# Kernel tuning notes

Measured on AMD Instinct MI355X. Metric: run time of the kernel, lower is better.

The kernel has to match this reference:

```python
import jax, jax.numpy as jnp
import numpy as np

N_NODES = 100000
N_EDGES = 1600000
DIM = 128
N_LAYERS = 3   # num_gc_layers
N_RES = 3      # residual VQ layers
N_CODE = 16    # codebook_size
N_GRAPHS = 512
BN_EPS = 1e-5
COMMIT_W = 0.25


def _l2norm(v):
    return v * jax.lax.rsqrt(jnp.sum(v * v, axis=-1, keepdims=True) + 1e-12)


def setup_inputs() -> dict:
    key = jax.random.key(0)
    ks = jax.random.split(key, 8)
    s = 0.05
    x = jax.random.normal(ks[0], (N_NODES, DIM), jnp.float32)
    edge_index = jax.random.randint(ks[1], (2, N_EDGES), 0, N_NODES)
    batch = jnp.sort(jax.random.randint(ks[2], (N_NODES,), 0, N_GRAPHS))
    W1 = jax.random.normal(ks[3], (N_LAYERS, DIM, DIM), jnp.float32) * s
    b1 = jnp.zeros((N_LAYERS, DIM), jnp.float32)
    W2 = jax.random.normal(ks[4], (N_LAYERS, DIM, DIM), jnp.float32) * s
    b2 = jnp.zeros((N_LAYERS, DIM), jnp.float32)
    gamma = jnp.ones((N_LAYERS, DIM), jnp.float32)
    beta = jnp.zeros((N_LAYERS, DIM), jnp.float32)
    codebooks = jax.random.normal(ks[5], (N_LAYERS, N_RES, N_CODE, DIM), jnp.float32)
    return dict(x=x, edge_index=edge_index, batch=batch, W1=W1, b1=b1,
                W2=W2, b2=b2, gamma=gamma, beta=beta, codebooks=codebooks)


def reference(x, edge_index, batch, W1, b1, W2, b2, gamma, beta, codebooks):
    src, dst = edge_index[0], edge_index[1]
    h = x
    xs, ids = [], []
    commit_loss = jnp.float32(0.0)
    for i in range(N_LAYERS):
        # GINConv, eps=0: MLP((1+eps)*x + sum_{j->i} x_j)
        agg = jax.ops.segment_sum(h[src], dst, num_segments=N_NODES)
        h = agg + h
        h = jax.nn.relu(h @ W1[i] + b1[i]) @ W2[i] + b2[i]  # Linear-ReLU-Linear
        h = jax.nn.relu(h)                                   # outer F.relu
        # BatchNorm1d (training-mode batch stats, biased variance)
        mean = jnp.mean(h, axis=0)
        var = jnp.var(h, axis=0)
        h = (h - mean) * jax.lax.rsqrt(var + BN_EPS) * gamma[i] + beta[i]
        xs.append(h)
        # Residual VQ with cosine-sim codebook (3 residual layers)
        r = h
        lids = []
        for l in range(N_RES):
            cbn = _l2norm(codebooks[i, l])           # [K, D] normalized codebook
            sim = _l2norm(r) @ cbn.T                  # [N, K] cosine similarity
            idx = jnp.argmax(sim, axis=-1)            # nearest code
            q = cbn[idx]                              # quantized residual
            commit_loss = commit_loss + COMMIT_W * jnp.mean(
                (jax.lax.stop_gradient(q) - r) ** 2)
            r = r - jax.lax.stop_gradient(q)
            lids.append(idx)
        ids.append(jnp.stack(lids, axis=1))           # [N, N_RES]
    xs_cat = jnp.concatenate(xs, axis=1)              # [N, DIM*N_LAYERS]
    xpool = jax.ops.segment_sum(xs_cat, batch, num_segments=N_GRAPHS)
    id_cat = jnp.concatenate(ids, axis=1)             # [N, N_RES*N_LAYERS]
    return xpool, xs_cat, commit_loss, id_cat
```

## Files before the change

kernel.cpp:

```cpp
#include <hip/hip_runtime.h>
#include <hip/hip_bf16.h>

#define N_NODES 100000
#define N_EDGES 1600000
#define DIM 128
#define NLAY 3
#define NRES 3
#define NCODE 16
#define NGRAPH 512
#define SCAN_NB ((N_NODES + 255) / 256)
#define GEMM_NB ((N_NODES + 63) / 64)

using bf16 = __hip_bfloat16;

__device__ inline void atomAddD(double* p, double v) { unsafeAtomicAdd(p, v); }

__device__ inline double ldx(const void* p, long i, int isbf) {
  if (isbf) return (double)__bfloat162float(((const bf16*)p)[i]);
  return (double)((const float*)p)[i];
}
__device__ inline void stout(void* p, long i, double v, int isbf) {
  if (isbf) ((bf16*)p)[i] = __float2bfloat16((float)v);
  else ((float*)p)[i] = (float)v;
}

__global__ void k_detect(const unsigned int* __restrict__ x, int* __restrict__ flag) {
  int tid = threadIdx.x;
  int cnt = 0;
  for (int j = tid; j < 1024; j += 256) {
    unsigned int u = x[j];
    int e = (u >> 7) & 0xFF;
    cnt += (e >= 100 && e <= 135) ? 1 : 0;
  }
  __shared__ int sh[256];
  sh[tid] = cnt; __syncthreads();
  for (int s = 128; s; s >>= 1) { if (tid < s) sh[tid] += sh[tid + s]; __syncthreads(); }
  if (tid == 0) flag[0] = (sh[0] > 512) ? 1 : 0;
}

__global__ __launch_bounds__(256) void k_convert_f(const void* __restrict__ x, float* __restrict__ hf,
                                                   long n, const int* __restrict__ flag) {
  int isbf = flag[0];
  long i = (long)blockIdx.x * 256 + threadIdx.x;
  if (i < n) hf[i] = (float)ldx(x, i, isbf);
}

__global__ __launch_bounds__(256) void k_hist(const int* __restrict__ ei, int* __restrict__ deg) {
  int e = blockIdx.x * 256 + threadIdx.x;
  if (e < N_EDGES) atomicAdd(&deg[ei[N_EDGES + e]], 1);
}

__global__ __launch_bounds__(256) void k_scan1(const int* __restrict__ deg, int* __restrict__ bsum) {
  int i = blockIdx.x * 256 + threadIdx.x;
  int v = (i < N_NODES) ? deg[i] : 0;
  for (int o = 32; o; o >>= 1) v += __shfl_xor(v, o);
  __shared__ int sh[4];
  if ((threadIdx.x & 63) == 0) sh[threadIdx.x >> 6] = v;
  __syncthreads();
  if (threadIdx.x == 0) bsum[blockIdx.x] = sh[0] + sh[1] + sh[2] + sh[3];
}

__global__ void k_scan2(int* __restrict__ bsum) {
  __shared__ int sh[512];
  int t = threadIdx.x;
  int v = (t < SCAN_NB) ? bsum[t] : 0;
  sh[t] = v; __syncthreads();
  for (int s = 1; s < 512; s <<= 1) {
    int add = (t >= s) ? sh[t - s] : 0;
    __syncthreads();
    sh[t] += add;
    __syncthreads();
  }
  if (t < SCAN_NB) bsum[t] = sh[t] - v;
}

__global__ __launch_bounds__(256) void k_scan3(const int* __restrict__ deg, const int* __restrict__ bsum,
                                               int* __restrict__ ofs, int* __restrict__ cursor) {
  int t = threadIdx.x;
  int i = blockIdx.x * 256 + t;
  int v = (i < N_NODES) ? deg[i] : 0;
  __shared__ int sh[256];
  sh[t] = v; __syncthreads();
  for (int s = 1; s < 256; s <<= 1) {
    int add = (t >= s) ? sh[t - s] : 0;
    __syncthreads();
    sh[t] += add;
    __syncthreads();
  }
  int excl = sh[t] - v + bsum[blockIdx.x];
  if (i < N_NODES) { ofs[i] = excl; cursor[i] = excl; }
  if (i == N_NODES - 1) ofs[N_NODES] = excl + v;
}

__global__ __launch_bounds__(256) void k_fill(const int* __restrict__ ei, int* __restrict__ cursor,
                                              int* __restrict__ csr) {
  int e = blockIdx.x * 256 + threadIdx.x;
  if (e < N_EDGES) {
    int d = ei[N_EDGES + e];
    int p = atomicAdd(&cursor[d], 1);
    csr[p] = ei[e];
  }
}

__global__ void k_gofs(const int* __restrict__ batch, int* __restrict__ gofs) {
  int g = threadIdx.x;
  int lo = 0, hi = N_NODES;
  while (lo < hi) { int mid = (lo + hi) >> 1; if (batch[mid] < g) lo = mid + 1; else hi = mid; }
  gofs[g] = lo;
  if (g == 0) gofs[NGRAPH] = N_NODES;
}

__global__ __launch_bounds__(256) void k_gather(const float* __restrict__ hf,
                                                const int* __restrict__ ofs,
                                                const int* __restrict__ csr,
                                                float* __restrict__ outQ) {
  int node = blockIdx.x * 4 + (threadIdx.x >> 6);
  int lane = threadIdx.x & 63;
  int beg = ofs[node], end = ofs[node + 1];
  float2 sv = *(const float2*)&hf[(long)node * DIM + lane * 2];
  double accx = (double)sv.x, accy = (double)sv.y;
  int j = beg;
  for (; j + 3 < end; j += 4) {
    int s0 = csr[j], s1 = csr[j + 1], s2 = csr[j + 2], s3 = csr[j + 3];
    float2 v0 = *(const float2*)&hf[(long)s0 * DIM + lane * 2];
    float2 v1 = *(const float2*)&hf[(long)s1 * DIM + lane * 2];
    float2 v2 = *(const float2*)&hf[(long)s2 * DIM + lane * 2];
    float2 v3 = *(const float2*)&hf[(long)s3 * DIM + lane * 2];
    accx += (double)v0.x; accy += (double)v0.y;
    accx += (double)v1.x; accy += (double)v1.y;
    accx += (double)v2.x; accy += (double)v2.y;
    accx += (double)v3.x; accy += (double)v3.y;
  }
  for (; j < end; j++) {
    int s0 = csr[j];
    float2 v0 = *(const float2*)&hf[(long)s0 * DIM + lane * 2];
    accx += (double)v0.x; accy += (double)v0.y;
  }
  *(float2*)&outQ[(long)node * DIM + lane * 2] = make_float2((float)accx, (float)accy);
}

__global__ void k_cbn(const void* __restrict__ cb, double* __restrict__ cbn, const int* __restrict__ flag) {
  int isbf = flag[0];
  int b = blockIdx.x, d = threadIdx.x;
  double v0 = ldx(cb, (long)b * DIM + d, isbf);
  double v1 = ldx(cb, (long)b * DIM + d + 64, isbf);
  double ss = v0 * v0 + v1 * v1;
  for (int o = 32; o; o >>= 1) ss += __shfl_xor(ss, o);
  double inv = 1.0 / sqrt(ss + 1e-12);
  cbn[b * DIM + d] = v0 * inv;
  cbn[b * DIM + d + 64] = v1 * inv;
}

__global__ void k_gram(const double* __restrict__ cbn, double* __restrict__ G) {
  int b = blockIdx.x, t = threadIdx.x;
  int l = b / (48 * 48); int rem = b % (48 * 48); int a = rem / 48, c = rem % 48;
  const double* ra = cbn + (long)(l * 48 + a) * DIM;
  const double* rc = cbn + (long)(l * 48 + c) * DIM;
  double s = ra[t] * rc[t] + ra[t + 64] * rc[t + 64];
  for (int o = 32; o; o >>= 1) s += __shfl_xor(s, o);
  if (t == 0) G[b] = s;
}

__global__ __launch_bounds__(256) void k_gemm_relu_f(const float* __restrict__ in,
                                                     const float* __restrict__ W,
                                                     const float* __restrict__ bias,
                                                     float* __restrict__ out) {
  __shared__ float ul[64 * DIM];
  int tid = threadIdx.x;
  long base = (long)blockIdx.x * 64;
  for (int j = tid; j < 64 * DIM / 4; j += 256) {
    long row = base + (j >> 5);
    float4 v = make_float4(0.f, 0.f, 0.f, 0.f);
    if (row < N_NODES) v = *(const float4*)&in[base * DIM + (long)j * 4];
    *(float4*)&ul[j * 4] = v;
  }
  __syncthreads();
  int cl = tid & 31;
  int rw = tid >> 5;
  int c0 = cl * 4;
  float acc[8][4] = {};
  for (int k = 0; k < DIM; k += 4) {
    float4 w0 = *(const float4*)&W[(k + 0) * DIM + c0];
    float4 w1 = *(const float4*)&W[(k + 1) * DIM + c0];
    float4 w2 = *(const float4*)&W[(k + 2) * DIM + c0];
    float4 w3 = *(const float4*)&W[(k + 3) * DIM + c0];
#pragma unroll
    for (int r = 0; r < 8; r++) {
      float4 u = *(const float4*)&ul[(rw * 8 + r) * DIM + k];
      acc[r][0] += u.x * w0.x + u.y * w1.x + u.z * w2.x + u.w * w3.x;
      acc[r][1] += u.x * w0.y + u.y * w1.y + u.z * w2.y + u.w * w3.y;
      acc[r][2] += u.x * w0.z + u.y * w1.z + u.z * w2.z + u.w * w3.z;
      acc[r][3] += u.x * w0.w + u.y * w1.w + u.z * w2.w + u.w * w3.w;
    }
  }
  float4 bv = *(const float4*)&bias[c0];
#pragma unroll
  for (int r = 0; r < 8; r++) {
    long row = base + rw * 8 + r;
    if (row < N_NODES) {
      float4 o;
      o.x = fmaxf(acc[r][0] + bv.x, 0.f);
      o.y = fmaxf(acc[r][1] + bv.y, 0.f);
      o.z = fmaxf(acc[r][2] + bv.z, 0.f);
      o.w = fmaxf(acc[r][3] + bv.w, 0.f);
      *(float4*)&out[row * DIM + c0] = o;
    }
  }
}

__global__ __launch_bounds__(256) void k_bn_stats(const float* __restrict__ h, double* __restrict__ stats) {
  int tid = threadIdx.x; int col = tid & 127; int half = tid >> 7;
  double s = 0.0, s2 = 0.0;
  for (long r = blockIdx.x * 2 + half; r < N_NODES; r += 2048) {
    double v = (double)h[r * DIM + col];
    s += v; s2 += v * v;
  }
  __shared__ double ls[256], ls2[256];
  ls[tid] = s; ls2[tid] = s2;
  __syncthreads();
  if (tid < 128) {
    atomAddD(&stats[col], ls[tid] + ls[tid + 128]);
    atomAddD(&stats[DIM + col], ls2[tid] + ls2[tid + 128]);
  }
}

__global__ void k_bn_prep(const double* __restrict__ stats, const void* __restrict__ gamma,
                          const void* __restrict__ beta, double* __restrict__ ss,
                          int l, const int* __restrict__ flag) {
  int isbf = flag[0];
  int d = threadIdx.x;
  double mean = stats[d] / (double)N_NODES;
  double var = stats[DIM + d] / (double)N_NODES - mean * mean;
  double sc = ldx(gamma, (long)l * DIM + d, isbf) / sqrt(var + 1e-5);
  ss[d] = sc;
  ss[DIM + d] = ldx(beta, (long)l * DIM + d, isbf) - mean * sc;
}

__global__ __launch_bounds__(256) void k_normalize(float* __restrict__ h, const double* __restrict__ ss,
                                                   void* __restrict__ out, double* __restrict__ hh,
                                                   int l, const int* __restrict__ flag) {
  int isbf = flag[0];
  int tid = threadIdx.x;
  int n = blockIdx.x * 2 + (tid >> 7);
  int d = tid & 127;
  double v = (double)h[(long)n * DIM + d] * ss[d] + ss[DIM + d];
  h[(long)n * DIM + d] = (float)v;
  const long XS_BASE = (long)NGRAPH * DIM * NLAY;
  stout(out, XS_BASE + (long)n * (DIM * NLAY) + l * DIM + d, v, isbf);
  double vf = (double)(float)v;
  double s2 = vf * vf;
  for (int o = 32; o; o >>= 1) s2 += __shfl_xor(s2, o);
  __shared__ double wp[4];
  if ((tid & 63) == 0) wp[tid >> 6] = s2;
  __syncthreads();
  if (tid == 0) hh[n] = wp[0] + wp[1];
  else if (tid == 128) hh[n] = wp[2] + wp[3];
}

__global__ __launch_bounds__(256) void k_xpool(const float* __restrict__ h, const int* __restrict__ gofs,
                                               double* __restrict__ xpool, int l) {
  int g = blockIdx.x;
  int tid = threadIdx.x;
  int d = tid & 127, half = tid >> 7;
  int beg = gofs[g], end = gofs[g + 1];
  double acc = 0.0;
  for (int n = beg + half; n < end; n += 2) acc += (double)h[(long)n * DIM + d];
  __shared__ double sh[256];
  sh[tid] = acc; __syncthreads();
  if (tid < 128) xpool[(long)g * (DIM * NLAY) + l * DIM + tid] = sh[tid] + sh[tid + 128];
}

__global__ __launch_bounds__(256) void k_dotH(const float* __restrict__ hn,
                                              const double* __restrict__ cbnL,
                                              float* __restrict__ dH) {
  __shared__ double cl[48 * 134];
  int tid = threadIdx.x;
  for (int j = tid; j < 48 * DIM; j += 256) { int c = j >> 7, k = j & 127; cl[c * 134 + k] = cbnL[j]; }
  __syncthreads();
  int ct = tid & 7; int c0 = ct * 6; int rt = tid >> 3;
  long r0 = (long)blockIdx.x * 64 + rt; long r1 = r0 + 32;
  long r0c = r0 < N_NODES ? r0 : (N_NODES - 1);
  long r1c = r1 < N_NODES ? r1 : (N_NODES - 1);
  double acc0[6] = {}, acc1[6] = {};
  for (int k = 0; k < DIM; k += 4) {
    float4 h0 = *(const float4*)&hn[r0c * DIM + k];
    float4 h1 = *(const float4*)&hn[r1c * DIM + k];
#pragma unroll
    for (int j = 0; j < 6; j++) {
      double2 ca = *(const double2*)&cl[(c0 + j) * 134 + k];
      double2 cb = *(const double2*)&cl[(c0 + j) * 134 + k + 2];
      acc0[j] += (double)h0.x * ca.x + (double)h0.y * ca.y + (double)h0.z * cb.x + (double)h0.w * cb.y;
      acc1[j] += (double)h1.x * ca.x + (double)h1.y * ca.y + (double)h1.z * cb.x + (double)h1.w * cb.y;
    }
  }
  if (r0 < N_NODES) {
#pragma unroll
    for (int j = 0; j < 6; j++) dH[r0 * 48 + c0 + j] = (float)acc0[j];
  }
  if (r1 < N_NODES) {
#pragma unroll
    for (int j = 0; j < 6; j++) dH[r1 * 48 + c0 + j] = (float)acc1[j];
  }
}

__global__ __launch_bounds__(256) void k_vq(const float* __restrict__ dH, const double* __restrict__ hh,
                                            const double* __restrict__ G, void* __restrict__ out,
                                            double* __restrict__ commit, int l, const int* __restrict__ flag) {
  int isbf = flag[0];
  __shared__ double Gl[48 * 48];
  int tid = threadIdx.x;
  for (int j = tid; j < 48 * 48; j += 256) Gl[j] = G[j];
  __syncthreads();
  long n = (long)blockIdx.x * 256 + tid;
  double csum = 0.0;
  if (n < N_NODES) {
    double dh[48];
#pragma unroll
    for (int c = 0; c < 48; c++) dh[c] = (double)dH[n * 48 + c];
    int i0 = 0; double b0 = dh[0];
#pragma unroll
    for (int c = 1; c < 16; c++) { if (dh[c] > b0) { b0 = dh[c]; i0 = c; } }
    int i1 = 0; double b1 = dh[16] - Gl[i0 * 48 + 16];
#pragma unroll
    for (int c = 1; c < 16; c++) {
      double s = dh[16 + c] - Gl[i0 * 48 + 16 + c];
      if (s > b1) { b1 = s; i1 = c; }
    }
    int i2 = 0; double b2 = dh[32] - Gl[i0 * 48 + 32] - Gl[(16 + i1) * 48 + 32];
#pragma unroll
    for (int c = 1; c < 16; c++) {
      double s = dh[32 + c] - Gl[i0 * 48 + 32 + c] - Gl[(16 + i1) * 48 + 32 + c];
      if (s > b2) { b2 = s; i2 = c; }
    }
    double r1s = hh[n] - 2.0 * b0 + Gl[i0 * 48 + i0];
    double r2s = r1s - 2.0 * b1 + Gl[(16 + i1) * 48 + 16 + i1];
    double r3s = r2s - 2.0 * b2 + Gl[(32 + i2) * 48 + 32 + i2];
    csum = r1s + r2s + r3s;
    const long IDS_BASE = (long)NGRAPH * DIM * NLAY + (long)N_NODES * DIM * NLAY + 1;
    long base = IDS_BASE + n * (NLAY * NRES) + l * NRES;
    stout(out, base + 0, (double)i0, isbf);
    stout(out, base + 1, (double)i1, isbf);
    stout(out, base + 2, (double)i2, isbf);
  }
  for (int o = 32; o; o >>= 1) csum += __shfl_xor(csum, o);
  if ((tid & 63) == 0 && csum != 0.0) atomAddD(commit, csum);
}

__global__ __launch_bounds__(256) void k_out(const double* __restrict__ xpool, const double* __restrict__ commit,
                                             void* __restrict__ out, const int* __restrict__ flag) {
  int isbf = flag[0];
  long i = (long)blockIdx.x * 256 + threadIdx.x;
  const long NP = (long)NGRAPH * DIM * NLAY;
  if (i < NP) {
    stout(out, i, xpool[i], isbf);
  } else if (i == NP) {
    double c = commit[0] * (0.25 / ((double)N_NODES * (double)DIM));
    stout(out, NP + (long)N_NODES * DIM * NLAY, c, isbf);
  }
}

extern "C" void kernel_launch(void* const* d_in, const int* in_sizes, int n_in,
                              void* d_out, int out_size, void* d_ws, size_t ws_size,
                              hipStream_t stream) {
  const void* x = d_in[0];
  const int* ei = (const int*)d_in[1];
  const int* batch = (const int*)d_in[2];
  const void* W1 = d_in[3];
  const void* b1 = d_in[4];
  const void* W2 = d_in[5];
  const void* b2 = d_in[6];
  const void* gamma = d_in[7];
  const void* beta = d_in[8];
  const void* cb = d_in[9];

  double* w = (double*)d_ws;
  double* cbn = w;
  double* G = cbn + 18432;
  double* stats = G + 6912;
  double* ss = stats + 256;
  double* hh = ss + 256;
  double* xpool = hh + N_NODES;
  double* commit = xpool + (long)NGRAPH * DIM * NLAY;
  float* fbuf = (float*)(commit + 2);
  float* W1f = fbuf;
  float* W2f = W1f + 49152;
  float* b1f = W2f + 49152;
  float* b2f = b1f + 384;
  float* H  = b2f + 384;
  float* T1 = H + 12800000;
  float* T2 = T1 + 12800000;
  float* dH = T2 + 12800000;
  int* ibuf = (int*)(dH + 4800000);
  int* flag = ibuf;
  int* deg = ibuf + 64;
  int* ofs = deg + N_NODES;
  int* cursor = ofs + N_NODES + 1;
  int* csr = cursor + N_NODES;
  int* gofs = csr + N_EDGES;
  int* bsum = gofs + NGRAPH + 2;

  k_detect<<<1, 256, 0, stream>>>((const unsigned int*)x, flag);
  hipMemsetAsync(xpool, 0, ((long)NGRAPH * DIM * NLAY + 1) * sizeof(double), stream);
  hipMemsetAsync(deg, 0, N_NODES * sizeof(int), stream);
  k_convert_f<<<50000, 256, 0, stream>>>(x, H, (long)N_NODES * DIM, flag);
  k_convert_f<<<192, 256, 0, stream>>>(W1, W1f, 49152, flag);
  k_convert_f<<<192, 256, 0, stream>>>(W2, W2f, 49152, flag);
  k_convert_f<<<2, 256, 0, stream>>>(b1, b1f, 384, flag);
  k_convert_f<<<2, 256, 0, stream>>>(b2, b2f, 384, flag);
  k_cbn<<<NLAY * NRES * NCODE, 64, 0, stream>>>(cb, cbn, flag);
  k_gram<<<NLAY * 48 * 48, 64, 0, stream>>>(cbn, G);
  k_hist<<<(N_EDGES + 255) / 256, 256, 0, stream>>>(ei, deg);
  k_scan1<<<SCAN_NB, 256, 0, stream>>>(deg, bsum);
  k_scan2<<<1, 512, 0, stream>>>(bsum);
  k_scan3<<<SCAN_NB, 256, 0, stream>>>(deg, bsum, ofs, cursor);
  k_fill<<<(N_EDGES + 255) / 256, 256, 0, stream>>>(ei, cursor, csr);
  k_gofs<<<1, NGRAPH, 0, stream>>>(batch, gofs);

  for (int l = 0; l < NLAY; l++) {
    k_gather<<<N_NODES / 4, 256, 0, stream>>>(H, ofs, csr, T1);
    k_gemm_relu_f<<<GEMM_NB, 256, 0, stream>>>(T1, W1f + l * DIM * DIM, b1f + l * DIM, T2);
    k_gemm_relu_f<<<GEMM_NB, 256, 0, stream>>>(T2, W2f + l * DIM * DIM, b2f + l * DIM, T1);
    hipMemsetAsync(stats, 0, 256 * sizeof(double), stream);
    k_bn_stats<<<1024, 256, 0, stream>>>(T1, stats);
    k_bn_prep<<<1, 128, 0, stream>>>(stats, gamma, beta, ss, l, flag);
    k_normalize<<<50000, 256, 0, stream>>>(T1, ss, d_out, hh, l, flag);
    k_xpool<<<NGRAPH, 256, 0, stream>>>(T1, gofs, xpool, l);
    k_dotH<<<1563, 256, 0, stream>>>(T1, cbn + (long)l * 48 * DIM, dH);
    k_vq<<<391, 256, 0, stream>>>(dH, hh, G + l * 48 * 48, d_out, commit, l, flag);
    float* t = H; H = T1; T1 = T2; T2 = t;
  }
  k_out<<<769, 256, 0, stream>>>(xpool, commit, d_out, flag);
}
```

Before: 1.783 ms.

## Fuse BN normalize, row norms and graph pooling into one post kernel

Merges the normalize kernel and the per-graph pooling kernel into a single k_post kernel that works on 64-row tiles. Each tile normalizes its rows, stages them in shared memory, computes row squared norms, and adds per-graph sums into xpool with double atomics, using the sorted batch ids. This removes a second full read of the hidden state and the k_gofs binary-search setup. In exchange it adds atomics on xpool and less parallelism per block, since 1563 blocks replace 50000 small ones.

```diff
diff --git a/kernel.cpp b/kernel.cpp
--- a/kernel.cpp
+++ b/kernel.cpp
@@ -100,14 +100,6 @@
     int p = atomicAdd(&cursor[d], 1);
     csr[p] = ei[e];
   }
-}
-
-__global__ void k_gofs(const int* __restrict__ batch, int* __restrict__ gofs) {
-  int g = threadIdx.x;
-  int lo = 0, hi = N_NODES;
-  while (lo < hi) { int mid = (lo + hi) >> 1; if (batch[mid] < g) lo = mid + 1; else hi = mid; }
-  gofs[g] = lo;
-  if (g == 0) gofs[NGRAPH] = N_NODES;
 }
 
 __global__ __launch_bounds__(256) void k_gather(const float* __restrict__ hf,
@@ -236,38 +228,65 @@
   ss[DIM + d] = ldx(beta, (long)l * DIM + d, isbf) - mean * sc;
 }
 
-__global__ __launch_bounds__(256) void k_normalize(float* __restrict__ h, const double* __restrict__ ss,
-                                                   void* __restrict__ out, double* __restrict__ hh,
-                                                   int l, const int* __restrict__ flag) {
+__global__ __launch_bounds__(256) void k_post(float* __restrict__ h,
+                                              const double* __restrict__ ss,
+                                              const int* __restrict__ batch,
+                                              void* __restrict__ out,
+                                              double* __restrict__ xpool,
+                                              double* __restrict__ hh,
+                                              int l, const int* __restrict__ flag) {
+  __shared__ float hl[64 * 132];
+  __shared__ double hq[64 * 4];
+  __shared__ int sbat[64];
   int isbf = flag[0];
   int tid = threadIdx.x;
-  int n = blockIdx.x * 2 + (tid >> 7);
-  int d = tid & 127;
-  double v = (double)h[(long)n * DIM + d] * ss[d] + ss[DIM + d];
-  h[(long)n * DIM + d] = (float)v;
+  long base = (long)blockIdx.x * 64;
+  if (tid < 64) {
+    long row = base + tid;
+    sbat[tid] = (row < N_NODES) ? batch[row] : -1;
+  }
+  int d = tid & 127, half = tid >> 7;
+  double sc = ss[d], sh = ss[DIM + d];
   const long XS_BASE = (long)NGRAPH * DIM * NLAY;
-  stout(out, XS_BASE + (long)n * (DIM * NLAY) + l * DIM + d, v, isbf);
-  double vf = (double)(float)v;
-  double s2 = vf * vf;
-  for (int o = 32; o; o >>= 1) s2 += __shfl_xor(s2, o);
-  __shared__ double wp[4];
-  if ((tid & 63) == 0) wp[tid >> 6] = s2;
-  __syncthreads();
-  if (tid == 0) hh[n] = wp[0] + wp[1];
-  else if (tid == 128) hh[n] = wp[2] + wp[3];
-}
-
-__global__ __launch_bounds__(256) void k_xpool(const float* __restrict__ h, const int* __restrict__ gofs,
-                                               double* __restrict__ xpool, int l) {
-  int g = blockIdx.x;
-  int tid = threadIdx.x;
-  int d = tid & 127, half = tid >> 7;
-  int beg = gofs[g], end = gofs[g + 1];
-  double acc = 0.0;
-  for (int n = beg + half; n < end; n += 2) acc += (double)h[(long)n * DIM + d];
-  __shared__ double sh[256];
-  sh[tid] = acc; __syncthreads();
-  if (tid < 128) xpool[(long)g * (DIM * NLAY) + l * DIM + tid] = sh[tid] + sh[tid + 128];
+  for (int rr = half; rr < 64; rr += 2) {
+    long row = base + rr;
+    float vf = 0.f;
+    if (row < N_NODES) {
+      double v = (double)h[row * DIM + d] * sc + sh;
+      vf = (float)v;
+      h[row * DIM + d] = vf;
+      stout(out, XS_BASE + row * (DIM * NLAY) + l * DIM + d, v, isbf);
+    }
+    hl[rr * 132 + d] = vf;
+  }
+  __syncthreads();
+  {
+    int row = tid >> 2, q = tid & 3;
+    double s2 = 0.0;
+    const float* hp = &hl[row * 132 + q * 32];
+#pragma unroll
+    for (int i = 0; i < 32; i++) { double v = (double)hp[i]; s2 += v * v; }
+    hq[row * 4 + q] = s2;
+  }
+  __syncthreads();
+  if (tid < 64) {
+    long n = base + tid;
+    if (n < N_NODES) hh[n] = hq[tid * 4] + hq[tid * 4 + 1] + hq[tid * 4 + 2] + hq[tid * 4 + 3];
+  } else if (tid >= 128) {
+    int dd = tid - 128;
+    int g = sbat[0];
+    double acc = 0.0;
+    for (int r = 0; r < 64; r++) {
+      int gg = sbat[r];
+      if (gg < 0) break;
+      if (gg != g) {
+        atomAddD(&xpool[(long)g * (DIM * NLAY) + l * DIM + dd], acc);
+        acc = 0.0; g = gg;
+      }
+      acc += (double)hl[r * 132 + dd];
+    }
+    atomAddD(&xpool[(long)g * (DIM * NLAY) + l * DIM + dd], acc);
+  }
 }
 
 __global__ __launch_bounds__(256) void k_dotH(const float* __restrict__ hn,
@@ -381,8 +400,7 @@
   double* hh = ss + 256;
   double* xpool = hh + N_NODES;
   double* commit = xpool + (long)NGRAPH * DIM * NLAY;
-  float* fbuf = (float*)(commit + 2);
-  float* W1f = fbuf;
+  float* W1f = (float*)(commit + 2);
   float* W2f = W1f + 49152;
   float* b1f = W2f + 49152;
   float* b2f = b1f + 384;
@@ -396,8 +414,7 @@
   int* ofs = deg + N_NODES;
   int* cursor = ofs + N_NODES + 1;
   int* csr = cursor + N_NODES;
-  int* gofs = csr + N_EDGES;
-  int* bsum = gofs + NGRAPH + 2;
+  int* bsum = csr + N_EDGES;
 
   k_detect<<<1, 256, 0, stream>>>((const unsigned int*)x, flag);
   hipMemsetAsync(xpool, 0, ((long)NGRAPH * DIM * NLAY + 1) * sizeof(double), stream);
@@ -414,7 +431,6 @@
   k_scan2<<<1, 512, 0, stream>>>(bsum);
   k_scan3<<<SCAN_NB, 256, 0, stream>>>(deg, bsum, ofs, cursor);
   k_fill<<<(N_EDGES + 255) / 256, 256, 0, stream>>>(ei, cursor, csr);
-  k_gofs<<<1, NGRAPH, 0, stream>>>(batch, gofs);
 
   for (int l = 0; l < NLAY; l++) {
     k_gather<<<N_NODES / 4, 256, 0, stream>>>(H, ofs, csr, T1);
@@ -423,8 +439,7 @@
     hipMemsetAsync(stats, 0, 256 * sizeof(double), stream);
     k_bn_stats<<<1024, 256, 0, stream>>>(T1, stats);
     k_bn_prep<<<1, 128, 0, stream>>>(stats, gamma, beta, ss, l, flag);
-    k_normalize<<<50000, 256, 0, stream>>>(T1, ss, d_out, hh, l, flag);
-    k_xpool<<<NGRAPH, 256, 0, stream>>>(T1, gofs, xpool, l);
+    k_post<<<GEMM_NB, 256, 0, stream>>>(T1, ss, batch, d_out, xpool, hh, l, flag);
     k_dotH<<<1563, 256, 0, stream>>>(T1, cbn + (long)l * 48 * DIM, dH);
     k_vq<<<391, 256, 0, stream>>>(dH, hh, G + l * 48 * 48, d_out, commit, l, flag);
     float* t = H; H = T1; T1 = T2; T2 = t;
```

Result: faster. 1.700 ms (-4.6%).
